# Performance work log

Measured on AMD Instinct MI355X. Metric: run time of the kernel, lower is better.

## Reference

```python
import jax, jax.numpy as jnp
import numpy as np

# Module config
T = 4.0          # distillation temperature (init arg)
NUM_BINS = 256   # number of unique quantized feature values present in the tensors
N, C, H, W = 64, 256, 32, 32
EPS = 1e-8


def setup_inputs() -> dict:
    key = jax.random.key(0)
    k1, k2 = jax.random.split(key)
    # Quantized features: integer-valued floats in [0, NUM_BINS). All 256 levels
    # appear w.h.p., so torch.unique(features).sort()[0] == arange(NUM_BINS).
    feat_s = jax.random.randint(k1, (N, C, H, W), 0, NUM_BINS).astype(jnp.float32)
    feat_t = jax.random.randint(k2, (N, C, H, W), 0, NUM_BINS).astype(jnp.float32)
    return {"feat_s": feat_s, "feat_t": feat_t}


def _feature_to_prob(features):
    # Replaces the original per-unique-value Python loop with one fused
    # scatter-add histogram. Values are exact integers, so equality-compare
    # counting == bincount on the integer cast.
    b = features.shape[0]
    idx = features.reshape(b, -1).astype(jnp.int32)              # [N, C*H*W]
    hist = jnp.zeros((b, NUM_BINS), jnp.float32)
    hist = hist.at[jnp.arange(b)[:, None], idx].add(1.0)         # [N, NUM_BINS]
    return jnp.log(hist + EPS)


def reference(feat_s, feat_t):
    prob_s = _feature_to_prob(feat_s)
    prob_t = _feature_to_prob(feat_t)
    p_s = jax.nn.log_softmax(prob_s / T, axis=1)                 # log-probs
    p_t = jax.nn.softmax(prob_t / T, axis=1)                     # probs
    # F.kl_div(log_input=p_s, target=p_t, size_average=False) = sum p_t*(log p_t - p_s)
    kl = jnp.sum(p_t * (jnp.log(p_t) - p_s))
    loss = kl * (T ** 2) / feat_s.shape[0]
    return loss
```

## Files before the change

kernel.cpp:

```cpp
#include <hip/hip_runtime.h>

#define NBATCH    64
#define BINS      256
#define PER_BATCH (256 * 32 * 32)
#define THREADS   512
#define CHUNKS    8
#define F4_PER_CHUNK (PER_BATCH / 4 / CHUNKS)

__global__ __launch_bounds__(THREADS, 4) void hist_kernel(
    const float* __restrict__ fs, const float* __restrict__ ft,
    int* __restrict__ ghist) {
  __shared__ unsigned sh[64 * 256];
  const int tid = threadIdx.x;

  uint4* shv = (uint4*)sh;
#pragma unroll
  for (int k = 0; k < 8; ++k) shv[k * THREADS + tid] = make_uint4(0, 0, 0, 0);
  __syncthreads();

  const int tb    = blockIdx.x >> 3;
  const int chunk = blockIdx.x & 7;
  const float* src   = (tb < NBATCH) ? fs : ft;
  const int    batch = tb & (NBATCH - 1);
  const float4* p = (const float4*)(src + (size_t)batch * PER_BATCH)
                    + (size_t)chunk * F4_PER_CHUNK;

  const unsigned colb = ((unsigned)tid >> 1) << 2;

#define PROC1(x) {                                        \
    int b = (int)(x);                                     \
    unsigned a = ((unsigned)(b >> 2) << 10) + colb;       \
    atomicAdd((unsigned*)((char*)sh + a),                 \
              1u << ((b & 3) << 3)); }
#define PROC4(v) { PROC1(v.x) PROC1(v.y) PROC1(v.z) PROC1(v.w) }

  float4 c0 = p[tid], c1 = p[tid + 512], c2 = p[tid + 1024], c3 = p[tid + 1536];
#pragma unroll
  for (int g = 1; g < 4; ++g) {
    float4 n0 = p[g * 2048 + tid],        n1 = p[g * 2048 + 512 + tid],
           n2 = p[g * 2048 + 1024 + tid], n3 = p[g * 2048 + 1536 + tid];
    PROC4(c0) PROC4(c1) PROC4(c2) PROC4(c3)
    c0 = n0; c1 = n1; c2 = n2; c3 = n3;
  }
  PROC4(c0) PROC4(c1) PROC4(c2) PROC4(c3)
  __syncthreads();

  if (tid < 256) {
    const int g = tid >> 2;
    const unsigned qbase = (unsigned)g * 256u + (unsigned)(tid & 3) * 64u;
    unsigned acc0 = 0, acc1 = 0;
#pragma unroll 4
    for (int j = 0; j < 64; ++j) {
      unsigned w = sh[qbase + ((j + tid) & 63)];
      acc0 += w & 0x00FF00FFu;
      acc1 += (w >> 8) & 0x00FF00FFu;
    }
    acc0 += __shfl_xor(acc0, 1);  acc0 += __shfl_xor(acc0, 2);
    acc1 += __shfl_xor(acc1, 1);  acc1 += __shfl_xor(acc1, 2);

    const int sub = tid & 3;
    unsigned cnt = (((sub & 1) ? acc1 : acc0) >> ((sub & 2) * 8)) & 0xFFFFu;
    atomicAdd(&ghist[tb * BINS + tid], (int)cnt);
  }
}

__global__ __launch_bounds__(256) void kl_batch(
    const int* __restrict__ ghist, double* __restrict__ partial) {
  __shared__ double reda[4], redb[4];
  const int n = blockIdx.x, tid = threadIdx.x;
  const int w = tid >> 6, lane = tid & 63;
  const int* hs = ghist + n * BINS;
  const int* ht = ghist + (NBATCH + n) * BINS;

  double ls = log((double)hs[tid] + 1e-8) * 0.25;
  double lt = log((double)ht[tid] + 1e-8) * 0.25;

  double ms = ls, mt = lt;
  for (int off = 32; off; off >>= 1) {
    ms = fmax(ms, __shfl_xor(ms, off));
    mt = fmax(mt, __shfl_xor(mt, off));
  }
  if (lane == 0) { reda[w] = ms; redb[w] = mt; }
  __syncthreads();
  ms = fmax(fmax(reda[0], reda[1]), fmax(reda[2], reda[3]));
  mt = fmax(fmax(redb[0], redb[1]), fmax(redb[2], redb[3]));
  __syncthreads();

  double ss = exp(ls - ms), st = exp(lt - mt);
  for (int off = 32; off; off >>= 1) {
    ss += __shfl_xor(ss, off);
    st += __shfl_xor(st, off);
  }
  if (lane == 0) { reda[w] = ss; redb[w] = st; }
  __syncthreads();
  ss = reda[0] + reda[1] + reda[2] + reda[3];
  st = redb[0] + redb[1] + redb[2] + redb[3];
  const double lse_s = ms + log(ss);
  const double lse_t = mt + log(st);

  const double lpt = lt - lse_t;
  const double lps = ls - lse_s;
  double term = exp(lpt) * (lpt - lps);
  for (int off = 32; off; off >>= 1) term += __shfl_xor(term, off);
  __syncthreads();
  if (lane == 0) reda[w] = term;
  __syncthreads();
  if (tid == 0) partial[n] = reda[0] + reda[1] + reda[2] + reda[3];
}

__global__ __launch_bounds__(64) void finalize(
    const double* __restrict__ partial, float* __restrict__ out) {
  double v = partial[threadIdx.x];
  for (int off = 32; off; off >>= 1) v += __shfl_xor(v, off);
  if (threadIdx.x == 0) out[0] = (float)(v * 0.25);
}

extern "C" void kernel_launch(void* const* d_in, const int* in_sizes, int n_in,
                              void* d_out, int out_size, void* d_ws, size_t ws_size,
                              hipStream_t stream) {
  const float* fs = (const float*)d_in[0];
  const float* ft = (const float*)d_in[1];
  int*    ghist   = (int*)d_ws;
  double* partial = (double*)((char*)d_ws + 2 * NBATCH * BINS * sizeof(int));

  hipMemsetAsync(d_ws, 0, (size_t)2 * NBATCH * BINS * sizeof(int), stream);

  hist_kernel<<<dim3(128 * CHUNKS), dim3(THREADS), 0, stream>>>(fs, ft, ghist);
  kl_batch<<<dim3(NBATCH), dim3(256), 0, stream>>>(ghist, partial);
  finalize<<<dim3(1), dim3(64), 0, stream>>>(partial, (float*)d_out);
}
```

Baseline: 152.8 us.

## Write per-chunk histograms without global atomics and shrink hist blocks

The histogram kernel now uses 256-thread blocks over 16 chunks per batch, with a 32KB shared histogram instead of 64KB. Each block stores its partial histogram directly to its own slot in the workspace rather than atomically adding into a zeroed global histogram. The KL kernel sums the 16 partials per bin itself. This removes the memset launch and the global atomics, and lets more blocks fit per CU. The cost is extra partial-histogram traffic and more reduction work in kl_batch.

Result: no change. 151.3 us (-1.0%).

```diff
diff --git a/kernel.cpp b/kernel.cpp
--- a/kernel.cpp
+++ b/kernel.cpp
@@ -3,14 +3,15 @@
 #define NBATCH    64
 #define BINS      256
 #define PER_BATCH (256 * 32 * 32)
-#define THREADS   512
-#define CHUNKS    8
+#define THREADS   256
+#define CHUNKS    16
 #define F4_PER_CHUNK (PER_BATCH / 4 / CHUNKS)
+#define F4_PER_THREAD (F4_PER_CHUNK / THREADS)
 
-__global__ __launch_bounds__(THREADS, 4) void hist_kernel(
+__global__ __launch_bounds__(THREADS, 5) void hist_kernel(
     const float* __restrict__ fs, const float* __restrict__ ft,
-    int* __restrict__ ghist) {
-  __shared__ unsigned sh[64 * 256];
+    int* __restrict__ phist) {
+  __shared__ unsigned sh[64 * 128];
   const int tid = threadIdx.x;
 
   uint4* shv = (uint4*)sh;
@@ -18,8 +19,8 @@
   for (int k = 0; k < 8; ++k) shv[k * THREADS + tid] = make_uint4(0, 0, 0, 0);
   __syncthreads();
 
-  const int tb    = blockIdx.x >> 3;
-  const int chunk = blockIdx.x & 7;
+  const int tb    = blockIdx.x >> 4;
+  const int chunk = blockIdx.x & 15;
   const float* src   = (tb < NBATCH) ? fs : ft;
   const int    batch = tb & (NBATCH - 1);
   const float4* p = (const float4*)(src + (size_t)batch * PER_BATCH)
@@ -29,51 +30,56 @@
 
 #define PROC1(x) {                                        \
     int b = (int)(x);                                     \
-    unsigned a = ((unsigned)(b >> 2) << 10) + colb;       \
+    unsigned a = ((unsigned)(b >> 2) << 9) + colb;        \
     atomicAdd((unsigned*)((char*)sh + a),                 \
               1u << ((b & 3) << 3)); }
 #define PROC4(v) { PROC1(v.x) PROC1(v.y) PROC1(v.z) PROC1(v.w) }
 
-  float4 c0 = p[tid], c1 = p[tid + 512], c2 = p[tid + 1024], c3 = p[tid + 1536];
+  float4 c[8];
 #pragma unroll
-  for (int g = 1; g < 4; ++g) {
-    float4 n0 = p[g * 2048 + tid],        n1 = p[g * 2048 + 512 + tid],
-           n2 = p[g * 2048 + 1024 + tid], n3 = p[g * 2048 + 1536 + tid];
-    PROC4(c0) PROC4(c1) PROC4(c2) PROC4(c3)
-    c0 = n0; c1 = n1; c2 = n2; c3 = n3;
+  for (int k = 0; k < 8; ++k) c[k] = p[k * THREADS + tid];
+#pragma unroll
+  for (int k = 0; k < 8; ++k) {
+    float4 n = p[(8 + k) * THREADS + tid];
+    PROC4(c[k])
+    c[k] = n;
   }
-  PROC4(c0) PROC4(c1) PROC4(c2) PROC4(c3)
+#pragma unroll
+  for (int k = 0; k < 8; ++k) PROC4(c[k])
   __syncthreads();
 
-  if (tid < 256) {
-    const int g = tid >> 2;
-    const unsigned qbase = (unsigned)g * 256u + (unsigned)(tid & 3) * 64u;
-    unsigned acc0 = 0, acc1 = 0;
+  const int g = tid >> 2;
+  const unsigned qbase = (unsigned)g * 128u + (unsigned)(tid & 3) * 32u;
+  unsigned acc0 = 0, acc1 = 0;
 #pragma unroll 4
-    for (int j = 0; j < 64; ++j) {
-      unsigned w = sh[qbase + ((j + tid) & 63)];
-      acc0 += w & 0x00FF00FFu;
-      acc1 += (w >> 8) & 0x00FF00FFu;
-    }
-    acc0 += __shfl_xor(acc0, 1);  acc0 += __shfl_xor(acc0, 2);
-    acc1 += __shfl_xor(acc1, 1);  acc1 += __shfl_xor(acc1, 2);
+  for (int j = 0; j < 32; ++j) {
+    unsigned w = sh[qbase + ((j + tid) & 31)];
+    acc0 += w & 0x00FF00FFu;
+    acc1 += (w >> 8) & 0x00FF00FFu;
+  }
+  acc0 += __shfl_xor(acc0, 1);  acc0 += __shfl_xor(acc0, 2);
+  acc1 += __shfl_xor(acc1, 1);  acc1 += __shfl_xor(acc1, 2);
 
-    const int sub = tid & 3;
-    unsigned cnt = (((sub & 1) ? acc1 : acc0) >> ((sub & 2) * 8)) & 0xFFFFu;
-    atomicAdd(&ghist[tb * BINS + tid], (int)cnt);
-  }
+  const int sub = tid & 3;
+  unsigned cnt = (((sub & 1) ? acc1 : acc0) >> ((sub & 2) * 8)) & 0xFFFFu;
+  phist[blockIdx.x * BINS + tid] = (int)cnt;
 }
 
 __global__ __launch_bounds__(256) void kl_batch(
-    const int* __restrict__ ghist, double* __restrict__ partial) {
+    const int* __restrict__ phist, double* __restrict__ partial) {
   __shared__ double reda[4], redb[4];
   const int n = blockIdx.x, tid = threadIdx.x;
   const int w = tid >> 6, lane = tid & 63;
-  const int* hs = ghist + n * BINS;
-  const int* ht = ghist + (NBATCH + n) * BINS;
 
-  double ls = log((double)hs[tid] + 1e-8) * 0.25;
-  double lt = log((double)ht[tid] + 1e-8) * 0.25;
+  int hs = 0, ht = 0;
+#pragma unroll
+  for (int c = 0; c < CHUNKS; ++c) {
+    hs += phist[(n * CHUNKS + c) * BINS + tid];
+    ht += phist[((NBATCH + n) * CHUNKS + c) * BINS + tid];
+  }
+
+  double ls = log((double)hs + 1e-8) * 0.25;
+  double lt = log((double)ht + 1e-8) * 0.25;
 
   double ms = ls, mt = lt;
   for (int off = 32; off; off >>= 1) {
@@ -120,12 +126,10 @@
                               hipStream_t stream) {
   const float* fs = (const float*)d_in[0];
   const float* ft = (const float*)d_in[1];
-  int*    ghist   = (int*)d_ws;
-  double* partial = (double*)((char*)d_ws + 2 * NBATCH * BINS * sizeof(int));
+  int*    phist   = (int*)d_ws;
+  double* partial = (double*)((char*)d_ws + (size_t)128 * CHUNKS * BINS * sizeof(int));
 
-  hipMemsetAsync(d_ws, 0, (size_t)2 * NBATCH * BINS * sizeof(int), stream);
-
-  hist_kernel<<<dim3(128 * CHUNKS), dim3(THREADS), 0, stream>>>(fs, ft, ghist);
-  kl_batch<<<dim3(NBATCH), dim3(256), 0, stream>>>(ghist, partial);
+  hist_kernel<<<dim3(128 * CHUNKS), dim3(THREADS), 0, stream>>>(fs, ft, phist);
+  kl_batch<<<dim3(NBATCH), dim3(256), 0, stream>>>(phist, partial);
   finalize<<<dim3(1), dim3(64), 0, stream>>>(partial, (float*)d_out);
 }
```
